# Kernel optimization log

Hardware: AMD Instinct MI355X
Metric: run time of the kernel (lower is better)

The kernel has to match this reference:

```python
import jax, jax.numpy as jnp
import numpy as np

EPS = 1e-8

def squash(t, axis=-1):
    sq = jnp.sum(t * t, axis=axis, keepdims=True)
    scale = sq / (1.0 + sq)
    return scale * t / jnp.sqrt(sq + EPS)

def setup_inputs() -> dict:
    key = jax.random.key(0)
    k1, k2 = jax.random.split(key)
    B, N_IN, D_IN, N_OUT, D_OUT = 256, 1152, 8, 10, 16
    x = jax.random.normal(k1, (B, N_IN, D_IN), dtype=jnp.float32)
    W = 0.01 * jax.random.normal(k2, (1, N_IN, N_OUT, D_OUT, D_IN), dtype=jnp.float32)
    return {"x": x, "W": W}

def reference(x, W):
    # u_hat[b,n,o,j] = sum_i W[0,n,o,j,i] * x[b,n,i]   -> (B, N_in, N_out, D_out)
    u_hat = jnp.einsum('noji,bni->bnoj', W[0], x)
    # b_ij starts with batch dim 1 (as in original torch code) and broadcasts
    b_ij = jnp.zeros((1, u_hat.shape[1], u_hat.shape[2], 1), dtype=u_hat.dtype)
    v_j = None
    for _ in range(3):  # fixed 3 routing iterations
        c_ij = jax.nn.softmax(b_ij, axis=2)            # over output capsules
        s_j = jnp.sum(c_ij * u_hat, axis=1, keepdims=True)  # (B,1,N_out,D_out)
        v_j = squash(s_j, axis=-1)
        b_ij = b_ij + jnp.sum(u_hat * v_j, axis=-1, keepdims=True)
    return jnp.squeeze(v_j, axis=1)  # (B, N_out, D_out)
```

## Files before the change

### kernel.cpp

```cpp
#include <hip/hip_runtime.h>

#define B_ 256
#define N_IN 1152
#define N_OUT 10
#define D_OUT 16
#define OJ 160
#define SN (B_*OJ)
#define LOG2E 1.44269504088896340736f
#define NPB 16
#define NPW 4
#define NSG (N_IN/NPB)

typedef __attribute__((ext_vector_type(8))) short bf16x8;
typedef __attribute__((ext_vector_type(4))) float f32x4;

#define NW_ELEMS (N_IN*N_OUT*D_OUT)
#define NX_ELEMS (B_*N_IN)
#define NWB (NW_ELEMS/256)
#define NTILES ((N_IN/16)*(B_/16))

__device__ __forceinline__ unsigned short f2bf(float f) {
  unsigned u = __float_as_uint(f);
  u += 0x7fffu + ((u >> 16) & 1u);
  return (unsigned short)(u >> 16);
}
__device__ __forceinline__ float bf2f(unsigned short s) {
  return __uint_as_float(((unsigned)s) << 16);
}
__device__ __forceinline__ void split8(const float* p, bf16x8& vh, bf16x8& vl) {
  const float4 a = *(const float4*)p;
  const float4 b = *(const float4*)(p + 4);
  const float w[8] = {a.x,a.y,a.z,a.w,b.x,b.y,b.z,b.w};
#pragma unroll
  for (int e=0;e<8;e++){
    unsigned short hh = f2bf(w[e]);
    vh[e] = (short)hh;
    vl[e] = (short)f2bf(w[e] - bf2f(hh));
  }
}

template<int CTRL>
__device__ __forceinline__ float dpp_add(float xx) {
  int y = __builtin_amdgcn_mov_dpp(__float_as_int(xx), CTRL, 0xF, 0xF, false);
  return xx + __int_as_float(y);
}
__device__ __forceinline__ float row_sum16(float xx) {
  xx = dpp_add<0x128>(xx); xx = dpp_add<0x124>(xx);
  xx = dpp_add<0x122>(xx); xx = dpp_add<0x121>(xx);
  return xx;
}
__device__ __forceinline__ float squash_elem(float t) {
  const float sq = row_sum16(t * t);
  return t * (sq / (1.f + sq)) * rsqrtf(sq + 1e-8f);
}

__global__ __launch_bounds__(256) void pack_all(const float* __restrict__ W,
                                                const float* __restrict__ x,
                                                short* __restrict__ WH, short* __restrict__ WL,
                                                short* __restrict__ XH, short* __restrict__ XL) {
  const int bid = blockIdx.x, tid = threadIdx.x;
  if (bid < NWB) {
    const int t = bid*256 + tid;
    bf16x8 vh, vl; split8(W + (size_t)t*8, vh, vl);
    ((bf16x8*)WH)[t] = vh; ((bf16x8*)WL)[t] = vl;
  } else {
    __shared__ bf16x8 TH[16*17], TL[16*17];
    const int tile = bid - NWB;
    const int nt = tile >> 4, bt = tile & 15;
    const int nn = tid & 15, bb = tid >> 4;
    bf16x8 vh, vl;
    split8(x + ((size_t)(bt*16+bb)*N_IN + nt*16+nn)*8, vh, vl);
    TH[nn*17 + bb] = vh; TL[nn*17 + bb] = vl;
    __syncthreads();
    const int bb2 = tid & 15, nn2 = tid >> 4;
    const size_t o = (size_t)(nt*16+nn2)*B_ + bt*16 + bb2;
    ((bf16x8*)XH)[o] = TH[nn2*17 + bb2];
    ((bf16x8*)XL)[o] = TL[nn2*17 + bb2];
  }
}


__global__ __launch_bounds__(256) void caps_pass1(const short* __restrict__ WH,
                                                  const short* __restrict__ WL,
                                                  const short* __restrict__ XH,
                                                  const short* __restrict__ XL,
                                                  float* __restrict__ P) {
  __shared__ f32x4 red[3*640];
  const int tid = threadIdx.x, w = tid >> 6, l = tid & 63;
  const int bb = l & 15, c = l >> 4;
  const int b0 = blockIdx.y * 16;
  const int n0 = blockIdx.x * NPB + w * NPW;
  const short* Abase = (c & 1)  ? WL : WH;
  const short* Bbase = (c >> 1) ? XL : XH;

  f32x4 acc[N_OUT];
  const f32x4 zz = {0.f,0.f,0.f,0.f};
#pragma unroll
  for (int o=0;o<N_OUT;o++) acc[o] = zz;

  for (int nn=0; nn<NPW; ++nn) {
    const int n = n0 + nn;
    const bf16x8 bfrag = *(const bf16x8*)&Bbase[((size_t)n*B_ + b0 + bb)*8];
    const short* Ap = &Abase[(size_t)n*1280 + bb*8];
#pragma unroll
    for (int o=0;o<N_OUT;o++) {
      const bf16x8 afrag = *(const bf16x8*)&Ap[o*128];
      acc[o] = __builtin_amdgcn_mfma_f32_16x16x32_bf16(afrag, bfrag, acc[o], 0,0,0);
    }
  }

  if (w) {
#pragma unroll
    for (int o=0;o<N_OUT;o++) red[(w-1)*640 + o*64 + l] = acc[o];
  }
  __syncthreads();
  if (!w) {
    float* Pp = &P[((size_t)blockIdx.x*B_ + b0 + bb)*OJ + c*4];
#pragma unroll
    for (int o=0;o<N_OUT;o++) {
      acc[o] += red[o*64+l] + red[640+o*64+l] + red[1280+o*64+l];
      *(f32x4*)&Pp[o*16] = acc[o];
    }
  }
}

__global__ __launch_bounds__(256) void caps_pass23(const short* __restrict__ WH,
                                                   const short* __restrict__ WL,
                                                   const short* __restrict__ XH,
                                                   const short* __restrict__ XL,
                                                   const float* __restrict__ veff,
                                                   float* __restrict__ P) {
  __shared__ f32x4 red[3*640];
  const int tid = threadIdx.x, w = tid >> 6, l = tid & 63;
  const int bb = l & 15, c = l >> 4;
  const int b0 = blockIdx.y * 16;
  const int n0 = blockIdx.x * NPB + w * NPW;
  const short* Abase = (c & 1)  ? WL : WH;
  const short* Bbase = (c >> 1) ? XL : XH;

  f32x4 vj[N_OUT], acc[N_OUT];
  const f32x4 zz = {0.f,0.f,0.f,0.f};
  const float* vp = &veff[(size_t)(b0+bb)*OJ + c*4];
#pragma unroll
  for (int o=0;o<N_OUT;o++) { vj[o] = *(const f32x4*)&vp[o*16]; acc[o] = zz; }

  for (int nn=0; nn<NPW; ++nn) {
    const int n = n0 + nn;
    const bf16x8 bfrag = *(const bf16x8*)&Bbase[((size_t)n*B_ + b0 + bb)*8];
    const short* Ap = &Abase[(size_t)n*1280 + bb*8];
    f32x4 u[N_OUT];
#pragma unroll
    for (int o=0;o<N_OUT;o++) {
      const bf16x8 afrag = *(const bf16x8*)&Ap[o*128];
      u[o] = __builtin_amdgcn_mfma_f32_16x16x32_bf16(afrag, bfrag, zz, 0,0,0);
    }
    float ez[N_OUT], Z = 0.f;
#pragma unroll
    for (int o=0;o<N_OUT;o++) {
      float t = u[o][0]*vj[o][0] + u[o][1]*vj[o][1]
              + u[o][2]*vj[o][2] + u[o][3]*vj[o][3];
      t += __shfl_xor(t, 16);
      t += __shfl_xor(t, 32);
      ez[o] = exp2f(t);
      Z += ez[o];
    }
    const float invZ = __builtin_amdgcn_rcpf(Z);
#pragma unroll
    for (int o=0;o<N_OUT;o++) acc[o] += (ez[o] * invZ) * u[o];
  }

  if (w) {
#pragma unroll
    for (int o=0;o<N_OUT;o++) red[(w-1)*640 + o*64 + l] = acc[o];
  }
  __syncthreads();
  if (!w) {
    float* Pp = &P[((size_t)blockIdx.x*B_ + b0 + bb)*OJ + c*4];
#pragma unroll
    for (int o=0;o<N_OUT;o++) {
      acc[o] += red[o*64+l] + red[640+o*64+l] + red[1280+o*64+l];
      *(f32x4*)&Pp[o*16] = acc[o];
    }
  }
}

__global__ __launch_bounds__(256) void caps_finish(const float* __restrict__ P, float scale,
                                                   const float* __restrict__ vprev,
                                                   float* __restrict__ vout, float lscale) {
  const int idx = blockIdx.x*256 + threadIdx.x;
  float t = 0.f;
#pragma unroll 8
  for (int g=0; g<NSG; ++g) t += P[(size_t)g*SN + idx];
  t *= scale;
  float v = squash_elem(t) * lscale;
  if (vprev != nullptr) v += vprev[idx];
  vout[idx] = v;
}

extern "C" void kernel_launch(void* const* d_in, const int* in_sizes, int n_in,
                              void* d_out, int out_size, void* d_ws, size_t ws_size,
                              hipStream_t stream) {
  const float* x = (const float*)d_in[0];
  const float* W = (const float*)d_in[1];
  float* out = (float*)d_out;

  float* P   = (float*)d_ws;
  float* v1  = P  + (size_t)NSG*SN;
  float* v12 = v1 + SN;
  short* WH = (short*)(v12 + SN);
  short* WL = WH + (size_t)NW_ELEMS*8;
  short* XH = WL + (size_t)NW_ELEMS*8;
  short* XL = XH + (size_t)NX_ELEMS*8;

  pack_all<<<NWB + NTILES, 256, 0, stream>>>(W, x, WH, WL, XH, XL);

  const dim3 pg(NSG, 16), pb(256);

  caps_pass1<<<pg, pb, 0, stream>>>(WH, WL, XH, XL, P);
  caps_finish<<<SN/256, 256, 0, stream>>>(P, 0.1f, nullptr, v1, LOG2E);

  caps_pass23<<<pg, pb, 0, stream>>>(WH, WL, XH, XL, v1, P);
  caps_finish<<<SN/256, 256, 0, stream>>>(P, 1.0f, v1, v12, LOG2E);

  caps_pass23<<<pg, pb, 0, stream>>>(WH, WL, XH, XL, v12, P);
  caps_finish<<<SN/256, 256, 0, stream>>>(P, 1.0f, nullptr, out, 1.0f);
}
```

Baseline: 85.92 us.

## Fuse first routing pass into pack kernel using direct FP32 FMA

```diff
diff --git a/kernel.cpp b/kernel.cpp
--- a/kernel.cpp
+++ b/kernel.cpp
@@ -10,6 +10,7 @@
 #define NPB 16
 #define NPW 4
 #define NSG (N_IN/NPB)
+#define NP1BLK (NSG*16)
 
 typedef __attribute__((ext_vector_type(8))) short bf16x8;
 typedef __attribute__((ext_vector_type(4))) float f32x4;
@@ -54,18 +55,47 @@
   return t * (sq / (1.f + sq)) * rsqrtf(sq + 1e-8f);
 }
 
-__global__ __launch_bounds__(256) void pack_all(const float* __restrict__ W,
-                                                const float* __restrict__ x,
-                                                short* __restrict__ WH, short* __restrict__ WL,
-                                                short* __restrict__ XH, short* __restrict__ XL) {
+__global__ __launch_bounds__(256) void d1_fused(
+    const float* __restrict__ W, const float* __restrict__ x,
+    short* __restrict__ WH, short* __restrict__ WL,
+    short* __restrict__ XH, short* __restrict__ XL,
+    float* __restrict__ P) {
   const int bid = blockIdx.x, tid = threadIdx.x;
-  if (bid < NWB) {
-    const int t = bid*256 + tid;
+  if (bid < NP1BLK) {
+    const int sg = bid >> 4, bg = bid & 15;
+    const int bb = tid >> 4, j = tid & 15;
+    const int b = bg*16 + bb;
+    const int n0 = sg*NPB;
+
+    float acc[N_OUT];
+#pragma unroll
+    for (int o=0;o<N_OUT;o++) acc[o] = 0.f;
+
+    const float* xp = &x[((size_t)b*N_IN + n0)*8];
+    const float* Wp = &W[(size_t)n0*1280 + j*8];
+    for (int nn=0; nn<NPB; ++nn) {
+      const f32x4 xa = *(const f32x4*)xp;
+      const f32x4 xb = *(const f32x4*)(xp+4);
+#pragma unroll
+      for (int o=0;o<N_OUT;o++) {
+        const f32x4 wa = *(const f32x4*)(Wp + o*128);
+        const f32x4 wb = *(const f32x4*)(Wp + o*128 + 4);
+        acc[o] += wa.x*xa.x + wa.y*xa.y + wa.z*xa.z + wa.w*xa.w
+                + wb.x*xb.x + wb.y*xb.y + wb.z*xb.z + wb.w*xb.w;
+      }
+      xp += 8;
+      Wp += 1280;
+    }
+    float* Pp = &P[(size_t)sg*SN + (size_t)b*OJ + j];
+#pragma unroll
+    for (int o=0;o<N_OUT;o++) Pp[o*16] = acc[o];
+  } else if (bid < NP1BLK + NWB) {
+    const int t = (bid - NP1BLK)*256 + tid;
     bf16x8 vh, vl; split8(W + (size_t)t*8, vh, vl);
     ((bf16x8*)WH)[t] = vh; ((bf16x8*)WL)[t] = vl;
   } else {
     __shared__ bf16x8 TH[16*17], TL[16*17];
-    const int tile = bid - NWB;
+    const int tile = bid - NP1BLK - NWB;
     const int nt = tile >> 4, bt = tile & 15;
     const int nn = tid & 15, bb = tid >> 4;
     bf16x8 vh, vl;
@@ -79,50 +109,6 @@
   }
 }
 
-
-__global__ __launch_bounds__(256) void caps_pass1(const short* __restrict__ WH,
-                                                  const short* __restrict__ WL,
-                                                  const short* __restrict__ XH,
-                                                  const short* __restrict__ XL,
-                                                  float* __restrict__ P) {
-  __shared__ f32x4 red[3*640];
-  const int tid = threadIdx.x, w = tid >> 6, l = tid & 63;
-  const int bb = l & 15, c = l >> 4;
-  const int b0 = blockIdx.y * 16;
-  const int n0 = blockIdx.x * NPB + w * NPW;
-  const short* Abase = (c & 1)  ? WL : WH;
-  const short* Bbase = (c >> 1) ? XL : XH;
-
-  f32x4 acc[N_OUT];
-  const f32x4 zz = {0.f,0.f,0.f,0.f};
-#pragma unroll
-  for (int o=0;o<N_OUT;o++) acc[o] = zz;
-
-  for (int nn=0; nn<NPW; ++nn) {
-    const int n = n0 + nn;
-    const bf16x8 bfrag = *(const bf16x8*)&Bbase[((size_t)n*B_ + b0 + bb)*8];
-    const short* Ap = &Abase[(size_t)n*1280 + bb*8];
-#pragma unroll
-    for (int o=0;o<N_OUT;o++) {
-      const bf16x8 afrag = *(const bf16x8*)&Ap[o*128];
-      acc[o] = __builtin_amdgcn_mfma_f32_16x16x32_bf16(afrag, bfrag, acc[o], 0,0,0);
-    }
-  }
-
-  if (w) {
-#pragma unroll
-    for (int o=0;o<N_OUT;o++) red[(w-1)*640 + o*64 + l] = acc[o];
-  }
-  __syncthreads();
-  if (!w) {
-    float* Pp = &P[((size_t)blockIdx.x*B_ + b0 + bb)*OJ + c*4];
-#pragma unroll
-    for (int o=0;o<N_OUT;o++) {
-      acc[o] += red[o*64+l] + red[640+o*64+l] + red[1280+o*64+l];
-      *(f32x4*)&Pp[o*16] = acc[o];
-    }
-  }
-}
 
 __global__ __launch_bounds__(256) void caps_pass23(const short* __restrict__ WH,
                                                    const short* __restrict__ WL,
@@ -212,16 +198,10 @@
   short* XH = WL + (size_t)NW_ELEMS*8;
   short* XL = XH + (size_t)NX_ELEMS*8;
 
-  pack_all<<<NWB + NTILES, 256, 0, stream>>>(W, x, WH, WL, XH, XL);
-
-  const dim3 pg(NSG, 16), pb(256);
-
-  caps_pass1<<<pg, pb, 0, stream>>>(WH, WL, XH, XL, P);
+  d1_fused<<<NP1BLK + NWB + NTILES, 256, 0, stream>>>(W, x, WH, WL, XH, XL, P);
   caps_finish<<<SN/256, 256, 0, stream>>>(P, 0.1f, nullptr, v1, LOG2E);
-
-  caps_pass23<<<pg, pb, 0, stream>>>(WH, WL, XH, XL, v1, P);
+  caps_pass23<<<dim3(NSG,16), 256, 0, stream>>>(WH, WL, XH, XL, v1, P);
   caps_finish<<<SN/256, 256, 0, stream>>>(P, 1.0f, v1, v12, LOG2E);
-
-  caps_pass23<<<pg, pb, 0, stream>>>(WH, WL, XH, XL, v12, P);
+  caps_pass23<<<dim3(NSG,16), 256, 0, stream>>>(WH, WL, XH, XL, v12, P);
   caps_finish<<<SN/256, 256, 0, stream>>>(P, 1.0f, nullptr, out, 1.0f);
 }
```

Measured after the change: 119.2 us. 1.39x slower.
